# Kernel tuning notes

Measured on AMD Instinct MI355X. Metric: run time of the kernel, lower is better.

Reference implementation:

```python
import jax, jax.numpy as jnp
import numpy as np

NMS_THRESH = 0.3  # default nms_thresh in DetNet.predict


def setup_inputs() -> dict:
    key = jax.random.key(0)
    k1, k2, k3, k4 = jax.random.split(key, 4)
    W, N = 8, 1024
    det = jax.random.uniform(k1, (W, N, 5), dtype=jnp.float32)          # (conf, cx, cy, w, h) in [0,1)
    offsets = jax.random.uniform(k2, (W, 5), dtype=jnp.float32) * 0.5   # window offset vector (0, left, top, 0, 0)-like
    scales = jax.random.uniform(k3, (W, 5), dtype=jnp.float32) * 0.5 + 0.25  # window scale vector
    b = jax.random.uniform(k4, (W, 4), dtype=jnp.float32)
    # (valid_left, valid_right, valid_top, valid_bottom) with left<right, top<bottom
    bounds = jnp.stack([0.3 * b[:, 0], 0.7 + 0.3 * b[:, 1],
                        0.3 * b[:, 2], 0.7 + 0.3 * b[:, 3]], axis=-1)
    return {"det": det, "offsets": offsets, "scales": scales, "bounds": bounds}


def _pairwise_iou(boxes):
    # boxes: [M,4] in (x1,y1,x2,y2)
    x1, y1, x2, y2 = boxes[:, 0], boxes[:, 1], boxes[:, 2], boxes[:, 3]
    area = jnp.clip(x2 - x1, 0.0) * jnp.clip(y2 - y1, 0.0)              # [M]
    iw = jnp.clip(jnp.minimum(x2[:, None], x2[None, :]) - jnp.maximum(x1[:, None], x1[None, :]), 0.0)
    ih = jnp.clip(jnp.minimum(y2[:, None], y2[None, :]) - jnp.maximum(y1[:, None], y1[None, :]), 0.0)
    inter = iw * ih                                                     # [M,M]
    union = area[:, None] + area[None, :] - inter
    return inter / jnp.maximum(union, 1e-9)


def reference(det, offsets, scales, bounds):
    W, N, _ = det.shape
    M = W * N
    cx, cy = det[..., 1], det[..., 2]                                    # [W,N]
    left, right = bounds[:, 0:1], bounds[:, 1:2]
    top, bottom = bounds[:, 2:3], bounds[:, 3:4]
    valid = (cx < right) & (cx > left) & (cy < bottom) & (cy > top)      # [W,N] border mask
    # torch.addcmul(offset, d, scale) = offset + d * scale
    d = (offsets[:, None, :] + det * scales[:, None, :]).reshape(M, 5)
    valid = valid.reshape(M)
    scores = jnp.where(valid, d[:, 0], -1.0)                             # invalid boxes never kept
    order = jnp.argsort(-scores)                                         # descending confidence
    d_s = d[order]                                                       # [M,5]
    s_s = scores[order]
    # point_form: (cx,cy,w,h) -> (x1,y1,x2,y2)
    cxy, wh = d_s[:, 1:3], d_s[:, 3:5]
    boxes = jnp.concatenate([cxy - wh * 0.5, cxy + wh * 0.5], axis=-1)
    iou = jax.lax.stop_gradient(_pairwise_iou(boxes))                    # [M,M], suppression is non-diff
    s_c = jax.lax.stop_gradient(s_s)
    idx = jnp.arange(M)

    def body(i, keep):
        # suppressed if any kept higher-score box overlaps > thresh
        sup = jnp.any(keep & (idx < i) & (iou[:, i] > NMS_THRESH))
        return keep.at[i].set(jnp.logical_and(~sup, s_c[i] > 0.0))

    keep = jax.lax.fori_loop(0, M, body, jnp.ones((M,), dtype=bool))
    return d_s * keep[:, None].astype(d_s.dtype)                         # [M,5], suppressed rows zeroed
```

## Files before the change

kernel.cpp:

```cpp
#include <hip/hip_runtime.h>
#include <cstdint>


#define M_TOT 8192
#define NMS_T 0.3f

#define WS_BOX   65536
#define WS_D     196608
#define WS_VCNT  360448
#define WS_ZROW  393216
#define WS_MASK  524288

typedef unsigned long long u64t;

__device__ __forceinline__ uint32_t desc_key(float sv) {
    uint32_t u = __float_as_uint(sv);
    uint32_t m = (u & 0x80000000u) ? ~u : (u | 0x80000000u);
    return ~m;
}

__device__ __forceinline__ u64t rdl64(u64t v, int sl) {
    unsigned lo = (unsigned)__builtin_amdgcn_readlane((int)(unsigned)v, sl);
    unsigned hi = (unsigned)__builtin_amdgcn_readlane((int)(unsigned)(v >> 32), sl);
    return ((u64t)hi << 32) | lo;
}
__device__ __forceinline__ u64t rdfl64(u64t v) {
    unsigned lo = (unsigned)__builtin_amdgcn_readfirstlane((int)(unsigned)v);
    unsigned hi = (unsigned)__builtin_amdgcn_readfirstlane((int)(unsigned)(v >> 32));
    return ((u64t)hi << 32) | lo;
}

__device__ __forceinline__ int scatter_one(
    int i, int rank, u64t key,
    const float* __restrict__ det, const float* __restrict__ offsets,
    const float* __restrict__ scales,
    float4* __restrict__ boxes_srt, float* __restrict__ d_srt)
{
    uint32_t dkey = (uint32_t)(key >> 16);
    if (dkey >= 0x7FFFFFFFu) return 0;
    int g = i >> 10;
    float d0 = __fadd_rn(offsets[g*5+0], __fmul_rn(det[i*5+0], scales[g*5+0]));
    float d1 = __fadd_rn(offsets[g*5+1], __fmul_rn(det[i*5+1], scales[g*5+1]));
    float d2 = __fadd_rn(offsets[g*5+2], __fmul_rn(det[i*5+2], scales[g*5+2]));
    float d3 = __fadd_rn(offsets[g*5+3], __fmul_rn(det[i*5+3], scales[g*5+3]));
    float d4 = __fadd_rn(offsets[g*5+4], __fmul_rn(det[i*5+4], scales[g*5+4]));
    d_srt[rank*5+0] = d0; d_srt[rank*5+1] = d1; d_srt[rank*5+2] = d2;
    d_srt[rank*5+3] = d3; d_srt[rank*5+4] = d4;
    float hw = __fmul_rn(d3, 0.5f), hh = __fmul_rn(d4, 0.5f);
    boxes_srt[rank] = make_float4(__fsub_rn(d1, hw), __fsub_rn(d2, hh),
                                  __fadd_rn(d1, hw), __fadd_rn(d2, hh));
    return 1;
}

__global__ __launch_bounds__(256) void k2_rank(
    const float* __restrict__ det, const float* __restrict__ offsets,
    const float* __restrict__ scales, const float* __restrict__ bounds,
    float4* __restrict__ boxes_srt, float* __restrict__ d_srt,
    unsigned int* __restrict__ vcnt, u64t* __restrict__ zrow,
    float* __restrict__ out)
{
    __shared__ u64t skey[M_TOT];
    __shared__ float soff[40], sscl[40], sbnd[32];
    __shared__ int sTop;
    int t = threadIdx.x;
    int lane = t & 63;
    if (t == 0) sTop = 0;
    if (t < 40) { soff[t] = offsets[t]; sscl[t] = scales[t]; }
    if (t < 32) { sbnd[t] = bounds[t]; }
    if (blockIdx.x == 0 && t < 128) zrow[t] = 0ull;
    __syncthreads();

    #pragma unroll 4
    for (int s = 0; s < 32; ++s) {
        int u = s * 256 + t;
        int g = u >> 10;
        float raw_s = det[u * 5 + 0];
        float cx    = det[u * 5 + 1];
        float cy    = det[u * 5 + 2];
        float score = __fadd_rn(soff[g * 5 + 0], __fmul_rn(raw_s, sscl[g * 5 + 0]));
        bool valid = (cx < sbnd[g*4+1]) && (cx > sbnd[g*4+0]) &&
                     (cy < sbnd[g*4+3]) && (cy > sbnd[g*4+2]);
        float sv = valid ? score : -1.0f;
        uint32_t dk = desc_key(sv);
        bool push = dk < 0x7FFFFFFFu;
        u64t key = ((u64t)dk << 16) | (unsigned)u;
        u64t bal = __ballot(push);
        if (bal) {
            int lw = 0;
            if (lane == 0) lw = atomicAdd(&sTop, __popcll(bal));
            int wbase = __builtin_amdgcn_readfirstlane(lw);
            if (push) {
                int off = __popcll(bal & ((1ull << lane) - 1ull));
                skey[wbase + off] = key;
            }
        }
    }
    __syncthreads();
    int V = sTop;
    int Vpad = (V + 15) & ~15;
    if (t < Vpad - V) skey[V + t] = ~0ull;
    {
        int zb = blockIdx.x * 160;
        for (int z = zb + t; z < zb + 160; z += 256) out[z] = 0.0f;
    }
    __syncthreads();
    if (t == 0) *vcnt = (unsigned)V;

    int grp = t >> 3;
    int jq  = t & 7;
    int i = blockIdx.x * 32 + grp;
    int g = i >> 10;
    float raw_s = det[i * 5 + 0];
    float cx    = det[i * 5 + 1];
    float cy    = det[i * 5 + 2];
    float score = __fadd_rn(soff[g * 5 + 0], __fmul_rn(raw_s, sscl[g * 5 + 0]));
    bool valid = (cx < sbnd[g*4+1]) && (cx > sbnd[g*4+0]) &&
                 (cy < sbnd[g*4+3]) && (cy > sbnd[g*4+2]);
    float sv = valid ? score : -1.0f;
    uint32_t dk = desc_key(sv);
    u64t ki = ((u64t)dk << 16) | (unsigned)i;
    const ulonglong2* skey2 = (const ulonglong2*)skey;
    int c = 0;
    int nit = Vpad >> 4;
    #pragma unroll 4
    for (int it = 0; it < nit; ++it) {
        ulonglong2 kj = skey2[it * 8 + jq];
        c += (kj.x < ki) + (kj.y < ki);
    }
    c += __shfl_xor(c, 1);
    c += __shfl_xor(c, 2);
    c += __shfl_xor(c, 4);
    if (jq == 0)
        scatter_one(i, c, ki, det, offsets, scales, boxes_srt, d_srt);
}

__global__ __launch_bounds__(256) void k_mask(
    const float4* __restrict__ boxes_srt,
    const unsigned int* __restrict__ vcnt,
    u64t* __restrict__ mask)
{
    __shared__ float4 sb[16 * 65];
    __shared__ float  sa[16 * 65];
    int V = (int)*vcnt;
    int bx = blockIdx.x, by = blockIdx.y;
    if (bx * 32 >= V) return;
    if (by * 1024 >= V) return;
    if (by * 16 + 15 < (bx * 32) >> 6) return;
    int nc = (V + 63) >> 6;
    int tid = threadIdx.x;
    int cbase = by * 1024;
    for (int u = tid; u < 1024; u += 256) {
        float4 b = boxes_srt[cbase + u];
        int c = u >> 6, jj = u & 63;
        sb[c * 65 + jj] = b;
        sa[c * 65 + jj] = __fmul_rn(fmaxf(__fsub_rn(b.z, b.x), 0.0f),
                                    fmaxf(__fsub_rn(b.w, b.y), 0.0f));
    }
    __syncthreads();
    int r = bx * 32 + (tid >> 3);
    if (r >= V) return;
    float4 bi = boxes_srt[r];
    float ai = __fmul_rn(fmaxf(__fsub_rn(bi.z, bi.x), 0.0f),
                         fmaxf(__fsub_rn(bi.w, bi.y), 0.0f));
    int rw = r >> 6;
    #pragma unroll
    for (int k = 0; k < 2; ++k) {
        int wl = (tid & 7) + k * 8;
        int w = by * 16 + wl;
        if (w < rw || w >= nc) continue;
        u64t bits = 0;
        #pragma unroll 4
        for (int jj = 0; jj < 64; ++jj) {
            float4 bj = sb[wl * 65 + jj];
            float aj = sa[wl * 65 + jj];
            float iw = fmaxf(__fsub_rn(fminf(bi.z, bj.z), fmaxf(bi.x, bj.x)), 0.0f);
            float ih = fmaxf(__fsub_rn(fminf(bi.w, bj.w), fmaxf(bi.y, bj.y)), 0.0f);
            float inter = __fmul_rn(iw, ih);
            float uni   = __fsub_rn(__fadd_rn(ai, aj), inter);
            float iou   = __fdiv_rn(inter, fmaxf(uni, 1e-9f));
            int j = w * 64 + jj;
            if (j > r && iou > NMS_T) bits |= 1ull << jj;
        }
        mask[(size_t)r * 128 + w] = bits;
    }
}

struct WSlot { ulonglong2 dl, dh, n1l, n1h, n2l, n2h; };

__device__ __forceinline__ void fill_words(
    const u64t* __restrict__ mask, int lane, int T, WSlot& w)
{
    int rl = min(T * 128 + lane,      M_TOT - 1);
    int rh = min(T * 128 + 64 + lane, M_TOT - 1);
    const ulonglong2* mrl = (const ulonglong2*)(mask + (size_t)rl * 128);
    const ulonglong2* mrh = (const ulonglong2*)(mask + (size_t)rh * 128);
    int p0 = min(T,     63);
    int p1 = min(T + 1, 63);
    int p2 = min(T + 2, 63);
    w.dl  = mrl[p0]; w.dh  = mrh[p0];
    w.n1l = mrl[p1]; w.n1h = mrh[p1];
    w.n2l = mrl[p2]; w.n2h = mrh[p2];
}

__device__ __forceinline__ void res_step(
    const u64t* __restrict__ mask,
    u64t* sdead, u64t* ck, volatile int* res_prog, volatile int* h_prog,
    int lane, int nc, int T,
    u64t& cA_lo, u64t& cA_hi, u64t& cB_lo, u64t& cB_hi, WSlot& w)
{
    if (T >= 3) {
        int need = T - 2;
        while (true) {
            int hp = (lane < 7) ? h_prog[lane] : 0x7FFFFFFF;
            if (__ballot(hp < need) == 0ull) break;
        }
    }
    u64t dlo = rdfl64(((volatile u64t*)sdead)[2 * T]);
    u64t dhi = rdfl64(((volatile u64t*)sdead)[2 * T + 1]);
    u64t live_lo = ~(dlo | cA_lo);
    u64t live_hi = ~(dhi | cA_hi);
    u64t km_lo = 0, km_hi = 0;
    while (live_lo) {
        int bs = (int)__builtin_ctzll(live_lo);
        km_lo |= 1ull << bs;
        u64t rml = rdl64(w.dl.x, bs);
        u64t rmh = rdl64(w.dl.y, bs);
        live_lo &= ~rml & ~(1ull << bs);
        live_hi &= ~rmh;
    }
    while (live_hi) {
        int bs = (int)__builtin_ctzll(live_hi);
        km_hi |= 1ull << bs;
        u64t rmh = rdl64(w.dh.y, bs);
        live_hi &= ~rmh & ~(1ull << bs);
    }
    if (lane == 0) { ck[2 * T] = km_lo; ck[2 * T + 1] = km_hi; }
    __threadfence_block();
    if (lane == 0) *res_prog = T + 1;
    u64t c1l = 0, c1h = 0, c2l = 0, c2h = 0;
    u64t km = km_lo;
    while (km) {
        int b = (int)__builtin_ctzll(km); km &= km - 1;
        c1l |= rdl64(w.n1l.x, b); c1h |= rdl64(w.n1l.y, b);
        c2l |= rdl64(w.n2l.x, b); c2h |= rdl64(w.n2l.y, b);
    }
    km = km_hi;
    while (km) {
        int b = (int)__builtin_ctzll(km); km &= km - 1;
        c1l |= rdl64(w.n1h.x, b); c1h |= rdl64(w.n1h.y, b);
        c2l |= rdl64(w.n2h.x, b); c2h |= rdl64(w.n2h.y, b);
    }
    cA_lo = cB_lo | c1l; cA_hi = cB_hi | c1h;
    cB_lo = c2l;         cB_hi = c2h;
    fill_words(mask, lane, T + 3, w);
}

__global__ __launch_bounds__(512, 2) void k3_serial(
    const u64t* __restrict__ mask, const u64t* __restrict__ zrow,
    const float* __restrict__ d_srt, const unsigned int* __restrict__ vcnt,
    float* __restrict__ out)
{
    __shared__ u64t sdead[128];
    __shared__ u64t ck[128];
    __shared__ int  res_prog;
    __shared__ int  h_prog[7];
    int tid = threadIdx.x, wv = tid >> 6, lane = tid & 63;
    int V = (int)*vcnt;
    int nc = (V + 127) >> 7;
    if (tid < 128) {
        int bw = tid * 64;
        u64t w0 = 0;
        if (bw >= V)           w0 = ~0ull;
        else if (bw + 64 > V)  w0 = (~0ull) << (V - bw);
        sdead[tid] = w0;
        ck[tid] = 0ull;
    }
    if (tid == 0) res_prog = 0;
    if (tid < 7)  h_prog[tid] = tid;
    __syncthreads();

    if (wv == 0) {
        u64t cA_lo = 0, cA_hi = 0, cB_lo = 0, cB_hi = 0;
        WSlot WA, WB, WC;
        fill_words(mask, lane, 0, WA);
        fill_words(mask, lane, 1, WB);
        fill_words(mask, lane, 2, WC);
        for (int t = 0; t < nc; t += 3) {
            res_step(mask, sdead, ck, &res_prog, h_prog, lane, nc, t,
                     cA_lo, cA_hi, cB_lo, cB_hi, WA);
            if (t + 1 < nc)
                res_step(mask, sdead, ck, &res_prog, h_prog, lane, nc, t + 1,
                         cA_lo, cA_hi, cB_lo, cB_hi, WB);
            if (t + 2 < nc)
                res_step(mask, sdead, ck, &res_prog, h_prog, lane, nc, t + 2,
                         cA_lo, cA_hi, cB_lo, cB_hi, WC);
        }
    } else {
        int hh = wv - 1;
        for (int c = hh; c < nc; c += 7) {
            while (*(volatile int*)&res_prog <= c) __builtin_amdgcn_s_sleep(1);
            u64t kl = ((volatile u64t*)ck)[2 * c];
            u64t kh = ((volatile u64t*)ck)[2 * c + 1];
            if (kl | kh) {
                int base = c * 128;
                u64t ax = 0, ay = 0;
                while (kl | kh) {
                    ulonglong2 b[4];
                    #pragma unroll
                    for (int q = 0; q < 4; ++q) {
                        const ulonglong2* ptr;
                        if (kl) {
                            int b_ = __builtin_ctzll(kl); kl &= kl - 1;
                            ptr = (const ulonglong2*)(mask + (size_t)(base + b_) * 128) + lane;
                        } else if (kh) {
                            int b_ = __builtin_ctzll(kh); kh &= kh - 1;
                            ptr = (const ulonglong2*)(mask + (size_t)(base + 64 + b_) * 128) + lane;
                        } else {
                            ptr = (const ulonglong2*)zrow + lane;
                        }
                        b[q] = *ptr;
                    }
                    ax |= b[0].x | b[1].x | b[2].x | b[3].x;
                    ay |= b[0].y | b[1].y | b[2].y | b[3].y;
                }
                atomicOr(&sdead[2 * lane],     ax);
                atomicOr(&sdead[2 * lane + 1], ay);
            }
            __threadfence_block();
            if (lane == 0) ((volatile int*)h_prog)[hh] = c + 7;
        }
        if (lane == 0) ((volatile int*)h_prog)[hh] = 0x7FFFFFFF;
    }
    __syncthreads();
    if (tid < 128) {
        u64t m = ck[tid];
        while (m) {
            int b = __builtin_ctzll(m); m &= m - 1;
            int rr = tid * 64 + b;
            out[rr * 5 + 0] = d_srt[rr * 5 + 0];
            out[rr * 5 + 1] = d_srt[rr * 5 + 1];
            out[rr * 5 + 2] = d_srt[rr * 5 + 2];
            out[rr * 5 + 3] = d_srt[rr * 5 + 3];
            out[rr * 5 + 4] = d_srt[rr * 5 + 4];
        }
    }
}

extern "C" void kernel_launch(void* const* d_in, const int* in_sizes, int n_in,
                              void* d_out, int out_size, void* d_ws, size_t ws_size,
                              hipStream_t stream) {
    const float* det     = (const float*)d_in[0];
    const float* offsets = (const float*)d_in[1];
    const float* scales  = (const float*)d_in[2];
    const float* bounds  = (const float*)d_in[3];
    float* out = (float*)d_out;
    char* ws = (char*)d_ws;
    float4*       boxes = (float4*)(ws + WS_BOX);
    float*        d_srt = (float*)(ws + WS_D);
    unsigned int* vcnt  = (unsigned int*)(ws + WS_VCNT);
    u64t*         zrow  = (u64t*)(ws + WS_ZROW);
    u64t*         mask  = (u64t*)(ws + WS_MASK);

    k2_rank<<<256, 256, 0, stream>>>(det, offsets, scales, bounds, boxes, d_srt, vcnt, zrow, out);
    k_mask<<<dim3(256, 8), 256, 0, stream>>>(boxes, vcnt, mask);
    k3_serial<<<1, 512, 0, stream>>>(mask, zrow, d_srt, vcnt, out);
}
```

Baseline: 154.8 us.

## Fuse rank, mask and serial NMS kernels into one persistent kernel with grid barriers

Merges the three launches (rank/scatter, IoU mask, serial suppression) into a single persistent kernel of 128 blocks with 512 threads. Software grid barriers built on global atomics separate the phases, and block 0 runs the serial resolution at the end. The goal is to remove kernel launch gaps and inter-kernel drain. In exchange it adds a memset launch for the barrier counters, relies on all 128 blocks being co-resident, and runs the mask phase over fewer, larger blocks.

```diff
diff --git a/kernel.cpp b/kernel.cpp
--- a/kernel.cpp
+++ b/kernel.cpp
@@ -4,10 +4,11 @@
 
 #define M_TOT 8192
 #define NMS_T 0.3f
+#define NBLK  128
 
 #define WS_BOX   65536
 #define WS_D     196608
-#define WS_VCNT  360448
+#define WS_BAR   360448
 #define WS_ZROW  393216
 #define WS_MASK  524288
 
@@ -18,7 +19,6 @@
     uint32_t m = (u & 0x80000000u) ? ~u : (u | 0x80000000u);
     return ~m;
 }
-
 __device__ __forceinline__ u64t rdl64(u64t v, int sl) {
     unsigned lo = (unsigned)__builtin_amdgcn_readlane((int)(unsigned)v, sl);
     unsigned hi = (unsigned)__builtin_amdgcn_readlane((int)(unsigned)(v >> 32), sl);
@@ -30,14 +30,34 @@
     return ((u64t)hi << 32) | lo;
 }
 
-__device__ __forceinline__ int scatter_one(
+__device__ __forceinline__ void gbar(unsigned* cnt, unsigned* gen, int tid) {
+    __syncthreads();
+    if (tid == 0) {
+        unsigned g = __hip_atomic_load(gen, __ATOMIC_RELAXED, __HIP_MEMORY_SCOPE_AGENT);
+        __threadfence();
+        unsigned a = __hip_atomic_fetch_add(cnt, 1u, __ATOMIC_ACQ_REL,
+                                            __HIP_MEMORY_SCOPE_AGENT);
+        if (a + 1u == (unsigned)NBLK) {
+            __hip_atomic_store(cnt, 0u, __ATOMIC_RELAXED, __HIP_MEMORY_SCOPE_AGENT);
+            __hip_atomic_fetch_add(gen, 1u, __ATOMIC_RELEASE, __HIP_MEMORY_SCOPE_AGENT);
+        } else {
+            while (__hip_atomic_load(gen, __ATOMIC_ACQUIRE,
+                                     __HIP_MEMORY_SCOPE_AGENT) == g)
+                __builtin_amdgcn_s_sleep(2);
+        }
+        __threadfence();
+    }
+    __syncthreads();
+}
+
+__device__ __forceinline__ void scatter_one(
     int i, int rank, u64t key,
     const float* __restrict__ det, const float* __restrict__ offsets,
     const float* __restrict__ scales,
     float4* __restrict__ boxes_srt, float* __restrict__ d_srt)
 {
     uint32_t dkey = (uint32_t)(key >> 16);
-    if (dkey >= 0x7FFFFFFFu) return 0;
+    if (dkey >= 0x7FFFFFFFu) return;
     int g = i >> 10;
     float d0 = __fadd_rn(offsets[g*5+0], __fmul_rn(det[i*5+0], scales[g*5+0]));
     float d1 = __fadd_rn(offsets[g*5+1], __fmul_rn(det[i*5+1], scales[g*5+1]));
@@ -49,21 +69,96 @@
     float hw = __fmul_rn(d3, 0.5f), hh = __fmul_rn(d4, 0.5f);
     boxes_srt[rank] = make_float4(__fsub_rn(d1, hw), __fsub_rn(d2, hh),
                                   __fadd_rn(d1, hw), __fadd_rn(d2, hh));
-    return 1;
-}
-
-__global__ __launch_bounds__(256) void k2_rank(
+}
+
+struct WSlot { ulonglong2 dl, dh, n1l, n1h, n2l, n2h; };
+
+__device__ __forceinline__ void fill_words(
+    const u64t* __restrict__ mask, int lane, int T, WSlot& w)
+{
+    int rl = min(T * 128 + lane,      M_TOT - 1);
+    int rh = min(T * 128 + 64 + lane, M_TOT - 1);
+    const ulonglong2* mrl = (const ulonglong2*)(mask + (size_t)rl * 128);
+    const ulonglong2* mrh = (const ulonglong2*)(mask + (size_t)rh * 128);
+    int p0 = min(T, 63), p1 = min(T + 1, 63), p2 = min(T + 2, 63);
+    w.dl  = mrl[p0]; w.dh  = mrh[p0];
+    w.n1l = mrl[p1]; w.n1h = mrh[p1];
+    w.n2l = mrl[p2]; w.n2h = mrh[p2];
+}
+
+__device__ __forceinline__ void res_step(
+    const u64t* __restrict__ mask,
+    u64t* sdead, u64t* ck, volatile int* res_prog, volatile int* h_prog,
+    int lane, int T,
+    u64t& cA_lo, u64t& cA_hi, u64t& cB_lo, u64t& cB_hi, WSlot& w)
+{
+    if (T >= 3) {
+        int need = T - 2;
+        while (true) {
+            int hp = (lane < 7) ? h_prog[lane] : 0x7FFFFFFF;
+            if (__ballot(hp < need) == 0ull) break;
+        }
+    }
+    u64t dlo = rdfl64(((volatile u64t*)sdead)[2 * T]);
+    u64t dhi = rdfl64(((volatile u64t*)sdead)[2 * T + 1]);
+    u64t live_lo = ~(dlo | cA_lo);
+    u64t live_hi = ~(dhi | cA_hi);
+    u64t km_lo = 0, km_hi = 0;
+    while (live_lo) {
+        int bs = (int)__builtin_ctzll(live_lo);
+        km_lo |= 1ull << bs;
+        u64t rml = rdl64(w.dl.x, bs);
+        u64t rmh = rdl64(w.dl.y, bs);
+        live_lo &= ~rml & ~(1ull << bs);
+        live_hi &= ~rmh;
+    }
+    while (live_hi) {
+        int bs = (int)__builtin_ctzll(live_hi);
+        km_hi |= 1ull << bs;
+        u64t rmh = rdl64(w.dh.y, bs);
+        live_hi &= ~rmh & ~(1ull << bs);
+    }
+    if (lane == 0) { ck[2 * T] = km_lo; ck[2 * T + 1] = km_hi; }
+    __threadfence_block();
+    if (lane == 0) *res_prog = T + 1;
+    u64t c1l = 0, c1h = 0, c2l = 0, c2h = 0, km = km_lo;
+    while (km) {
+        int b = (int)__builtin_ctzll(km); km &= km - 1;
+        c1l |= rdl64(w.n1l.x, b); c1h |= rdl64(w.n1l.y, b);
+        c2l |= rdl64(w.n2l.x, b); c2h |= rdl64(w.n2l.y, b);
+    }
+    km = km_hi;
+    while (km) {
+        int b = (int)__builtin_ctzll(km); km &= km - 1;
+        c1l |= rdl64(w.n1h.x, b); c1h |= rdl64(w.n1h.y, b);
+        c2l |= rdl64(w.n2h.x, b); c2h |= rdl64(w.n2h.y, b);
+    }
+    cA_lo = cB_lo | c1l; cA_hi = cB_hi | c1h;
+    cB_lo = c2l;         cB_hi = c2h;
+    fill_words(mask, lane, T + 3, w);
+}
+
+__global__ __launch_bounds__(512) void k_all(
     const float* __restrict__ det, const float* __restrict__ offsets,
     const float* __restrict__ scales, const float* __restrict__ bounds,
     float4* __restrict__ boxes_srt, float* __restrict__ d_srt,
-    unsigned int* __restrict__ vcnt, u64t* __restrict__ zrow,
-    float* __restrict__ out)
+    u64t* __restrict__ zrow, u64t* __restrict__ mask,
+    unsigned* __restrict__ bar, float* __restrict__ out)
 {
     __shared__ u64t skey[M_TOT];
     __shared__ float soff[40], sscl[40], sbnd[32];
     __shared__ int sTop;
-    int t = threadIdx.x;
-    int lane = t & 63;
+    __shared__ float4 sb[16 * 65];
+    __shared__ float  sa[16 * 65];
+    __shared__ u64t sdead[128];
+    __shared__ u64t ck[128];
+    __shared__ int  res_prog;
+    __shared__ int  h_prog[7];
+
+    int t = threadIdx.x, lane = t & 63, wv = t >> 6;
+    unsigned* cnt = bar;
+    unsigned* gen = bar + 1;
+
     if (t == 0) sTop = 0;
     if (t < 40) { soff[t] = offsets[t]; sscl[t] = scales[t]; }
     if (t < 32) { sbnd[t] = bounds[t]; }
@@ -71,8 +166,8 @@
     __syncthreads();
 
     #pragma unroll 4
-    for (int s = 0; s < 32; ++s) {
-        int u = s * 256 + t;
+    for (int s = 0; s < 16; ++s) {
+        int u = s * 512 + t;
         int g = u >> 10;
         float raw_s = det[u * 5 + 0];
         float cx    = det[u * 5 + 1];
@@ -100,183 +195,101 @@
     int Vpad = (V + 15) & ~15;
     if (t < Vpad - V) skey[V + t] = ~0ull;
     {
-        int zb = blockIdx.x * 160;
-        for (int z = zb + t; z < zb + 160; z += 256) out[z] = 0.0f;
-    }
-    __syncthreads();
-    if (t == 0) *vcnt = (unsigned)V;
-
-    int grp = t >> 3;
-    int jq  = t & 7;
-    int i = blockIdx.x * 32 + grp;
-    int g = i >> 10;
-    float raw_s = det[i * 5 + 0];
-    float cx    = det[i * 5 + 1];
-    float cy    = det[i * 5 + 2];
-    float score = __fadd_rn(soff[g * 5 + 0], __fmul_rn(raw_s, sscl[g * 5 + 0]));
-    bool valid = (cx < sbnd[g*4+1]) && (cx > sbnd[g*4+0]) &&
-                 (cy < sbnd[g*4+3]) && (cy > sbnd[g*4+2]);
-    float sv = valid ? score : -1.0f;
-    uint32_t dk = desc_key(sv);
-    u64t ki = ((u64t)dk << 16) | (unsigned)i;
-    const ulonglong2* skey2 = (const ulonglong2*)skey;
-    int c = 0;
-    int nit = Vpad >> 4;
-    #pragma unroll 4
-    for (int it = 0; it < nit; ++it) {
-        ulonglong2 kj = skey2[it * 8 + jq];
-        c += (kj.x < ki) + (kj.y < ki);
-    }
-    c += __shfl_xor(c, 1);
-    c += __shfl_xor(c, 2);
-    c += __shfl_xor(c, 4);
-    if (jq == 0)
-        scatter_one(i, c, ki, det, offsets, scales, boxes_srt, d_srt);
-}
-
-__global__ __launch_bounds__(256) void k_mask(
-    const float4* __restrict__ boxes_srt,
-    const unsigned int* __restrict__ vcnt,
-    u64t* __restrict__ mask)
-{
-    __shared__ float4 sb[16 * 65];
-    __shared__ float  sa[16 * 65];
-    int V = (int)*vcnt;
-    int bx = blockIdx.x, by = blockIdx.y;
-    if (bx * 32 >= V) return;
-    if (by * 1024 >= V) return;
-    if (by * 16 + 15 < (bx * 32) >> 6) return;
-    int nc = (V + 63) >> 6;
-    int tid = threadIdx.x;
-    int cbase = by * 1024;
-    for (int u = tid; u < 1024; u += 256) {
-        float4 b = boxes_srt[cbase + u];
-        int c = u >> 6, jj = u & 63;
-        sb[c * 65 + jj] = b;
-        sa[c * 65 + jj] = __fmul_rn(fmaxf(__fsub_rn(b.z, b.x), 0.0f),
-                                    fmaxf(__fsub_rn(b.w, b.y), 0.0f));
-    }
-    __syncthreads();
-    int r = bx * 32 + (tid >> 3);
-    if (r >= V) return;
-    float4 bi = boxes_srt[r];
-    float ai = __fmul_rn(fmaxf(__fsub_rn(bi.z, bi.x), 0.0f),
-                         fmaxf(__fsub_rn(bi.w, bi.y), 0.0f));
-    int rw = r >> 6;
-    #pragma unroll
-    for (int k = 0; k < 2; ++k) {
-        int wl = (tid & 7) + k * 8;
-        int w = by * 16 + wl;
-        if (w < rw || w >= nc) continue;
-        u64t bits = 0;
+        int zb = blockIdx.x * 320;
+        for (int z = zb + t; z < zb + 320; z += 512) out[z] = 0.0f;
+    }
+    __syncthreads();
+
+    {
+        int grp = t >> 3, jq = t & 7;
+        int i = blockIdx.x * 64 + grp;
+        int g = i >> 10;
+        float raw_s = det[i * 5 + 0];
+        float cx    = det[i * 5 + 1];
+        float cy    = det[i * 5 + 2];
+        float score = __fadd_rn(soff[g * 5 + 0], __fmul_rn(raw_s, sscl[g * 5 + 0]));
+        bool valid = (cx < sbnd[g*4+1]) && (cx > sbnd[g*4+0]) &&
+                     (cy < sbnd[g*4+3]) && (cy > sbnd[g*4+2]);
+        float sv = valid ? score : -1.0f;
+        uint32_t dk = desc_key(sv);
+        u64t ki = ((u64t)dk << 16) | (unsigned)i;
+        const ulonglong2* skey2 = (const ulonglong2*)skey;
+        int c = 0;
+        int nit = Vpad >> 4;
         #pragma unroll 4
-        for (int jj = 0; jj < 64; ++jj) {
-            float4 bj = sb[wl * 65 + jj];
-            float aj = sa[wl * 65 + jj];
-            float iw = fmaxf(__fsub_rn(fminf(bi.z, bj.z), fmaxf(bi.x, bj.x)), 0.0f);
-            float ih = fmaxf(__fsub_rn(fminf(bi.w, bj.w), fmaxf(bi.y, bj.y)), 0.0f);
-            float inter = __fmul_rn(iw, ih);
-            float uni   = __fsub_rn(__fadd_rn(ai, aj), inter);
-            float iou   = __fdiv_rn(inter, fmaxf(uni, 1e-9f));
-            int j = w * 64 + jj;
-            if (j > r && iou > NMS_T) bits |= 1ull << jj;
-        }
-        mask[(size_t)r * 128 + w] = bits;
-    }
-}
-
-struct WSlot { ulonglong2 dl, dh, n1l, n1h, n2l, n2h; };
-
-__device__ __forceinline__ void fill_words(
-    const u64t* __restrict__ mask, int lane, int T, WSlot& w)
-{
-    int rl = min(T * 128 + lane,      M_TOT - 1);
-    int rh = min(T * 128 + 64 + lane, M_TOT - 1);
-    const ulonglong2* mrl = (const ulonglong2*)(mask + (size_t)rl * 128);
-    const ulonglong2* mrh = (const ulonglong2*)(mask + (size_t)rh * 128);
-    int p0 = min(T,     63);
-    int p1 = min(T + 1, 63);
-    int p2 = min(T + 2, 63);
-    w.dl  = mrl[p0]; w.dh  = mrh[p0];
-    w.n1l = mrl[p1]; w.n1h = mrh[p1];
-    w.n2l = mrl[p2]; w.n2h = mrh[p2];
-}
-
-__device__ __forceinline__ void res_step(
-    const u64t* __restrict__ mask,
-    u64t* sdead, u64t* ck, volatile int* res_prog, volatile int* h_prog,
-    int lane, int nc, int T,
-    u64t& cA_lo, u64t& cA_hi, u64t& cB_lo, u64t& cB_hi, WSlot& w)
-{
-    if (T >= 3) {
-        int need = T - 2;
-        while (true) {
-            int hp = (lane < 7) ? h_prog[lane] : 0x7FFFFFFF;
-            if (__ballot(hp < need) == 0ull) break;
-        }
-    }
-    u64t dlo = rdfl64(((volatile u64t*)sdead)[2 * T]);
-    u64t dhi = rdfl64(((volatile u64t*)sdead)[2 * T + 1]);
-    u64t live_lo = ~(dlo | cA_lo);
-    u64t live_hi = ~(dhi | cA_hi);
-    u64t km_lo = 0, km_hi = 0;
-    while (live_lo) {
-        int bs = (int)__builtin_ctzll(live_lo);
-        km_lo |= 1ull << bs;
-        u64t rml = rdl64(w.dl.x, bs);
-        u64t rmh = rdl64(w.dl.y, bs);
-        live_lo &= ~rml & ~(1ull << bs);
-        live_hi &= ~rmh;
-    }
-    while (live_hi) {
-        int bs = (int)__builtin_ctzll(live_hi);
-        km_hi |= 1ull << bs;
-        u64t rmh = rdl64(w.dh.y, bs);
-        live_hi &= ~rmh & ~(1ull << bs);
-    }
-    if (lane == 0) { ck[2 * T] = km_lo; ck[2 * T + 1] = km_hi; }
-    __threadfence_block();
-    if (lane == 0) *res_prog = T + 1;
-    u64t c1l = 0, c1h = 0, c2l = 0, c2h = 0;
-    u64t km = km_lo;
-    while (km) {
-        int b = (int)__builtin_ctzll(km); km &= km - 1;
-        c1l |= rdl64(w.n1l.x, b); c1h |= rdl64(w.n1l.y, b);
-        c2l |= rdl64(w.n2l.x, b); c2h |= rdl64(w.n2l.y, b);
-    }
-    km = km_hi;
-    while (km) {
-        int b = (int)__builtin_ctzll(km); km &= km - 1;
-        c1l |= rdl64(w.n1h.x, b); c1h |= rdl64(w.n1h.y, b);
-        c2l |= rdl64(w.n2h.x, b); c2h |= rdl64(w.n2h.y, b);
-    }
-    cA_lo = cB_lo | c1l; cA_hi = cB_hi | c1h;
-    cB_lo = c2l;         cB_hi = c2h;
-    fill_words(mask, lane, T + 3, w);
-}
-
-__global__ __launch_bounds__(512, 2) void k3_serial(
-    const u64t* __restrict__ mask, const u64t* __restrict__ zrow,
-    const float* __restrict__ d_srt, const unsigned int* __restrict__ vcnt,
-    float* __restrict__ out)
-{
-    __shared__ u64t sdead[128];
-    __shared__ u64t ck[128];
-    __shared__ int  res_prog;
-    __shared__ int  h_prog[7];
-    int tid = threadIdx.x, wv = tid >> 6, lane = tid & 63;
-    int V = (int)*vcnt;
+        for (int it = 0; it < nit; ++it) {
+            ulonglong2 kj = skey2[it * 8 + jq];
+            c += (kj.x < ki) + (kj.y < ki);
+        }
+        c += __shfl_xor(c, 1);
+        c += __shfl_xor(c, 2);
+        c += __shfl_xor(c, 4);
+        if (jq == 0)
+            scatter_one(i, c, ki, det, offsets, scales, boxes_srt, d_srt);
+    }
+
+    gbar(cnt, gen, t);
+
+    {
+        int ncw = (V + 63) >> 6;
+        for (int tile = blockIdx.x; tile < 128 * 8; tile += NBLK) {
+            int bx = tile >> 3, by = tile & 7;
+            if (bx * 64 >= V) continue;
+            if (by * 1024 >= V) continue;
+            if (by * 16 + 15 < (bx * 64) >> 6) continue;
+            __syncthreads();
+            int cbase = by * 1024;
+            for (int u = t; u < 1024; u += 512) {
+                float4 b = boxes_srt[cbase + u];
+                int c = u >> 6, jj = u & 63;
+                sb[c * 65 + jj] = b;
+                sa[c * 65 + jj] = __fmul_rn(fmaxf(__fsub_rn(b.z, b.x), 0.0f),
+                                            fmaxf(__fsub_rn(b.w, b.y), 0.0f));
+            }
+            __syncthreads();
+            int r = bx * 64 + (t >> 3);
+            if (r >= V) continue;
+            float4 bi = boxes_srt[r];
+            float ai = __fmul_rn(fmaxf(__fsub_rn(bi.z, bi.x), 0.0f),
+                                 fmaxf(__fsub_rn(bi.w, bi.y), 0.0f));
+            int rw = r >> 6;
+            #pragma unroll
+            for (int k = 0; k < 2; ++k) {
+                int wl = (t & 7) + k * 8;
+                int w = by * 16 + wl;
+                if (w < rw || w >= ncw) continue;
+                u64t bits = 0;
+                #pragma unroll 4
+                for (int jj = 0; jj < 64; ++jj) {
+                    float4 bj = sb[wl * 65 + jj];
+                    float aj = sa[wl * 65 + jj];
+                    float iw = fmaxf(__fsub_rn(fminf(bi.z, bj.z), fmaxf(bi.x, bj.x)), 0.0f);
+                    float ih = fmaxf(__fsub_rn(fminf(bi.w, bj.w), fmaxf(bi.y, bj.y)), 0.0f);
+                    float inter = __fmul_rn(iw, ih);
+                    float uni   = __fsub_rn(__fadd_rn(ai, aj), inter);
+                    float iou   = __fdiv_rn(inter, fmaxf(uni, 1e-9f));
+                    int j = w * 64 + jj;
+                    if (j > r && iou > NMS_T) bits |= 1ull << jj;
+                }
+                mask[(size_t)r * 128 + w] = bits;
+            }
+        }
+    }
+
+    gbar(cnt, gen, t);
+
+    if (blockIdx.x != 0) return;
     int nc = (V + 127) >> 7;
-    if (tid < 128) {
-        int bw = tid * 64;
+    if (t < 128) {
+        int bw = t * 64;
         u64t w0 = 0;
         if (bw >= V)           w0 = ~0ull;
         else if (bw + 64 > V)  w0 = (~0ull) << (V - bw);
-        sdead[tid] = w0;
-        ck[tid] = 0ull;
-    }
-    if (tid == 0) res_prog = 0;
-    if (tid < 7)  h_prog[tid] = tid;
+        sdead[t] = w0;
+        ck[t] = 0ull;
+    }
+    if (t == 0) res_prog = 0;
+    if (t < 7)  h_prog[t] = t;
     __syncthreads();
 
     if (wv == 0) {
@@ -285,14 +298,14 @@
         fill_words(mask, lane, 0, WA);
         fill_words(mask, lane, 1, WB);
         fill_words(mask, lane, 2, WC);
-        for (int t = 0; t < nc; t += 3) {
-            res_step(mask, sdead, ck, &res_prog, h_prog, lane, nc, t,
+        for (int T = 0; T < nc; T += 3) {
+            res_step(mask, sdead, ck, &res_prog, h_prog, lane, T,
                      cA_lo, cA_hi, cB_lo, cB_hi, WA);
-            if (t + 1 < nc)
-                res_step(mask, sdead, ck, &res_prog, h_prog, lane, nc, t + 1,
+            if (T + 1 < nc)
+                res_step(mask, sdead, ck, &res_prog, h_prog, lane, T + 1,
                          cA_lo, cA_hi, cB_lo, cB_hi, WB);
-            if (t + 2 < nc)
-                res_step(mask, sdead, ck, &res_prog, h_prog, lane, nc, t + 2,
+            if (T + 2 < nc)
+                res_step(mask, sdead, ck, &res_prog, h_prog, lane, T + 2,
                          cA_lo, cA_hi, cB_lo, cB_hi, WC);
         }
     } else {
@@ -332,11 +345,11 @@
         if (lane == 0) ((volatile int*)h_prog)[hh] = 0x7FFFFFFF;
     }
     __syncthreads();
-    if (tid < 128) {
-        u64t m = ck[tid];
+    if (t < 128) {
+        u64t m = ck[t];
         while (m) {
             int b = __builtin_ctzll(m); m &= m - 1;
-            int rr = tid * 64 + b;
+            int rr = t * 64 + b;
             out[rr * 5 + 0] = d_srt[rr * 5 + 0];
             out[rr * 5 + 1] = d_srt[rr * 5 + 1];
             out[rr * 5 + 2] = d_srt[rr * 5 + 2];
@@ -355,13 +368,13 @@
     const float* bounds  = (const float*)d_in[3];
     float* out = (float*)d_out;
     char* ws = (char*)d_ws;
-    float4*       boxes = (float4*)(ws + WS_BOX);
-    float*        d_srt = (float*)(ws + WS_D);
-    unsigned int* vcnt  = (unsigned int*)(ws + WS_VCNT);
-    u64t*         zrow  = (u64t*)(ws + WS_ZROW);
-    u64t*         mask  = (u64t*)(ws + WS_MASK);
-
-    k2_rank<<<256, 256, 0, stream>>>(det, offsets, scales, bounds, boxes, d_srt, vcnt, zrow, out);
-    k_mask<<<dim3(256, 8), 256, 0, stream>>>(boxes, vcnt, mask);
-    k3_serial<<<1, 512, 0, stream>>>(mask, zrow, d_srt, vcnt, out);
-}
+    float4*   boxes = (float4*)(ws + WS_BOX);
+    float*    d_srt = (float*)(ws + WS_D);
+    unsigned* bar   = (unsigned*)(ws + WS_BAR);
+    u64t*     zrow  = (u64t*)(ws + WS_ZROW);
+    u64t*     mask  = (u64t*)(ws + WS_MASK);
+
+    hipMemsetAsync(bar, 0, 2 * sizeof(unsigned), stream);
+    k_all<<<NBLK, 512, 0, stream>>>(det, offsets, scales, bounds,
+                                    boxes, d_srt, zrow, mask, bar, out);
+}
```

New measurement: 199.5 us. 1.29x slower.
